# Optimization experiments

Hardware: AMD Instinct MI355X
Metric: run time of the kernel (lower is better)

Reference implementation:

```python
import jax, jax.numpy as jnp
import numpy as np

CONF_THRESH = 0.01
TOP_K = 200        # per-class NMS candidate cap
NMS_THRESH = 0.45
KEEP_TOP_K = 200   # global per-image cap; also output K
TEMPERATURE = 1.0
V0, V1 = 0.1, 0.2  # variances


def _nms_keep(bxs, scs):
    """Greedy NMS over candidates sorted descending by score.
    bxs: [M,4] (x1,y1,x2,y2), scs: [M] (invalid slots have score -1).
    Returns keep mask [M] (bool). Matches torch nm_suppression: a box j is
    suppressed by kept box i iff NOT (IoU(i,j) <= thresh) (NaN IoU suppresses)."""
    x1, y1, x2, y2 = bxs[:, 0], bxs[:, 1], bxs[:, 2], bxs[:, 3]
    area = (x2 - x1) * (y2 - y1)
    xx1 = jnp.maximum(x1[:, None], x1[None, :])
    yy1 = jnp.maximum(y1[:, None], y1[None, :])
    xx2 = jnp.minimum(x2[:, None], x2[None, :])
    yy2 = jnp.minimum(y2[:, None], y2[None, :])
    inter = jnp.clip(xx2 - xx1, 0.0) * jnp.clip(yy2 - yy1, 0.0)
    union = area[None, :] - inter + area[:, None]  # row i: area[i] + area[j] - inter
    iou = inter / union  # [M,M]
    M = scs.shape[0]
    valid = scs > CONF_THRESH

    def step(active, i):
        k_i = active[i]                                  # kept iff still active (sorted desc)
        sup = k_i & jnp.logical_not(iou[i] <= NMS_THRESH)
        return active & jnp.logical_not(sup), k_i

    _, keep = jax.lax.scan(step, valid, jnp.arange(M))
    return keep


def _forward(loc_data, conf_data, dbox_list):
    B, N, C = conf_data.shape
    M, K = TOP_K, KEEP_TOP_K
    # --- box decode (SSD) ---
    db = dbox_list[None]                                   # [1,N,4]
    cxcy = db[..., :2] + loc_data[..., :2] * V0 * db[..., 2:]
    wh = db[..., 2:] * jnp.exp(loc_data[..., 2:] * V1)
    mins = cxcy - wh * 0.5
    boxes = jnp.clip(jnp.concatenate([mins, mins + wh], -1), 0.0, 1.0)  # [B,N,4]
    # --- class scores ---
    probs = jax.nn.softmax(conf_data / TEMPERATURE, axis=-1)
    sc = jnp.swapaxes(probs[..., 1:], 1, 2)                # [B,C-1,N] (skip background)
    masked = jnp.where(sc > CONF_THRESH, sc, -1.0)
    top_sc, top_idx = jax.lax.top_k(masked, M)             # [B,C-1,M] desc
    cand = jnp.take_along_axis(boxes[:, None], top_idx[..., None], axis=2)  # [B,C-1,M,4]
    # --- per-class greedy NMS ---
    keep = jax.vmap(jax.vmap(_nms_keep))(cand, top_sc)     # [B,C-1,M]
    kept_sc = jnp.where(keep, top_sc, 0.0)
    # --- global keep_top_k across classes (torch topk over concatenated dets) ---
    flat = kept_sc.reshape(B, -1)
    order = jnp.argsort(-flat, axis=1)
    rank = jnp.argsort(order, axis=1)                      # inverse permutation = desc rank
    keep_g = (flat > 0.0) & (rank < K)
    fin_sc = jnp.where(keep_g, flat, 0.0).reshape(B, C - 1, M)
    fin_bx = jnp.where(keep_g.reshape(B, C - 1, M)[..., None], cand, 0.0)
    # --- per-class compaction (stable desc sort keeps NMS order among survivors) ---
    ord2 = jnp.argsort(-fin_sc, axis=2)
    sc_out = jnp.take_along_axis(fin_sc, ord2, axis=2)[..., :K]
    bx_out = jnp.take_along_axis(fin_bx, ord2[..., None], axis=2)[..., :K, :]
    body = jnp.concatenate([sc_out[..., None], bx_out], axis=-1)  # [B,C-1,K,5]
    bg = jnp.zeros((B, 1, K, 5), body.dtype)               # class 0 (background) row stays 0
    return jnp.concatenate([bg, body], axis=1)             # [B,C,K,5]


def setup_inputs() -> dict:
    key = jax.random.key(0)
    k1, k2, k3 = jax.random.split(key, 3)
    B, N, C = 8, 32768, 81
    loc_data = jax.random.normal(k1, (B, N, 4), jnp.float32)
    conf_data = jax.random.normal(k2, (B, N, C), jnp.float32)
    dbox_list = jax.random.uniform(k3, (N, 4), jnp.float32, 0.05, 0.95)  # cx,cy,w,h priors
    return {"loc_data": loc_data, "conf_data": conf_data, "dbox_list": dbox_list}


def reference(loc_data, conf_data, dbox_list):
    return _forward(loc_data, conf_data, dbox_list)
```

## Files before the change

kernel.cpp:

```cpp
#include <hip/hip_runtime.h>
#include <stdint.h>

#define CONF_T 0.01f
#define NMS_T  0.45f
#define M_TOP  200
#define TK_BS  512
#define TCAP   2048

typedef float float4u __attribute__((ext_vector_type(4), aligned(4)));

__device__ __forceinline__ uint32_t fkey(float f) {
    uint32_t u = __float_as_uint(f);
    return (u & 0x80000000u) ? ~u : (u | 0x80000000u);
}
__device__ __forceinline__ float fkey_inv(uint32_t k) {
    uint32_t u = (k & 0x80000000u) ? (k & 0x7FFFFFFFu) : ~k;
    return __uint_as_float(u);
}

__device__ __forceinline__ void suffix_select(
        uint32_t* hist, uint32_t* wsum, int nb, uint32_t pref, int shift,
        uint32_t wantv, uint32_t* s_prefix, uint32_t* s_want) {
    int tid = threadIdx.x;
    int lane = tid & 63, w = tid >> 6;
    int bpt = nb >> 8;
    int base = tid * bpt;
    uint32_t loc = 0, sfx = 0;
    if (tid < 256) {
        for (int j = 0; j < bpt; j++) loc += hist[base + j];
        sfx = loc;
        #pragma unroll
        for (int d = 1; d < 64; d <<= 1) {
            uint32_t y = __shfl_down(sfx, d);
            if (lane + d < 64) sfx += y;
        }
        if (lane == 0) wsum[w] = sfx;
    }
    __syncthreads();
    if (tid < 256) {
        uint32_t later = 0;
        for (int j = w + 1; j < 4; j++) later += wsum[j];
        uint32_t run = (sfx - loc) + later;
        for (int j = bpt - 1; j >= 0; j--) {
            uint32_t h = hist[base + j];
            uint32_t s2 = run + h;
            if (run < wantv && s2 >= wantv) {
                *s_prefix = pref | ((uint32_t)(base + j) << shift);
                *s_want   = wantv - run;
            }
            run = s2;
        }
    }
    __syncthreads();
}

__device__ __forceinline__ void suffix_select2(
        uint32_t* hist, uint32_t* wsum, int nb, uint32_t want_a, uint32_t want_b,
        uint32_t* s_bin_a, uint32_t* s_bin_b) {
    int tid = threadIdx.x;
    int lane = tid & 63, w = tid >> 6;
    int bpt = nb >> 8;
    int base = tid * bpt;
    uint32_t loc = 0, sfx = 0;
    if (tid < 256) {
        for (int j = 0; j < bpt; j++) loc += hist[base + j];
        sfx = loc;
        #pragma unroll
        for (int d = 1; d < 64; d <<= 1) {
            uint32_t y = __shfl_down(sfx, d);
            if (lane + d < 64) sfx += y;
        }
        if (lane == 0) wsum[w] = sfx;
    }
    __syncthreads();
    if (tid < 256) {
        uint32_t later = 0;
        for (int j = w + 1; j < 4; j++) later += wsum[j];
        uint32_t run = (sfx - loc) + later;
        for (int j = bpt - 1; j >= 0; j--) {
            uint32_t h = hist[base + j];
            uint32_t s2 = run + h;
            if (run < want_a && s2 >= want_a) *s_bin_a = (uint32_t)(base + j);
            if (run < want_b && s2 >= want_b) *s_bin_b = (uint32_t)(base + j);
            run = s2;
        }
    }
    __syncthreads();
}

__device__ __forceinline__ float4 decode_box(float4 l, float4 d) {
    float cx = d.x + (l.x * 0.1f) * d.z;
    float cy = d.y + (l.y * 0.1f) * d.w;
    float w  = d.z * expf(l.z * 0.2f);
    float h  = d.w * expf(l.w * 0.2f);
    float x1 = cx - w * 0.5f, y1 = cy - h * 0.5f;
    float x2 = x1 + w, y2 = y1 + h;
    float4 o;
    o.x = fminf(fmaxf(x1, 0.f), 1.f);
    o.y = fminf(fmaxf(y1, 0.f), 1.f);
    o.z = fminf(fmaxf(x2, 0.f), 1.f);
    o.w = fminf(fmaxf(y2, 0.f), 1.f);
    return o;
}

__global__ __launch_bounds__(256, 4) void softmax_kernel(
        const float* __restrict__ conf, float* __restrict__ sc,
        int* __restrict__ pcnt, int B, int N, int C) {
    int r = blockIdx.x * blockDim.x + threadIdx.x;
    if (r < B) pcnt[r] = 0;
    if (r >= B * N) return;
    const float* p = conf + (size_t)r * 81;
    float v[81];
    #pragma unroll
    for (int i = 0; i < 20; i++) {
        float4u f = *(const float4u*)(p + 4 * i);
        v[4 * i] = f.x; v[4 * i + 1] = f.y; v[4 * i + 2] = f.z; v[4 * i + 3] = f.w;
    }
    v[80] = p[80];
    float m = v[0];
    #pragma unroll
    for (int c = 1; c < 81; c++) m = fmaxf(m, v[c]);
    float s = 0.f;
    #pragma unroll
    for (int c = 0; c < 81; c++) { float e = expf(v[c] - m); v[c] = e; s += e; }
    int b = r / N, n = r % N;
    float* obase = sc + ((size_t)b * (C - 1)) * N + n;
    #pragma unroll
    for (int c = 1; c < 81; c++) obase[(size_t)(c - 1) * N] = v[c] / s;
}

__global__ __launch_bounds__(TK_BS) void topk_kernel(
        const float* __restrict__ sc, const float* __restrict__ loc,
        const float* __restrict__ dbox,
        float* __restrict__ cand,
        float* __restrict__ cmpval, int* __restrict__ cmpidx,
        int* __restrict__ pcnt,
        int B, int N, int Cm1, int M) {
    const uint32_t KEYN1 = 0x407FFFFFu;
    const uint32_t BIN_N1 = KEYN1 >> 21;
    __shared__ __align__(16) uint32_t hist[2048];
    __shared__ __align__(16) uint32_t tk[TCAP];
    __shared__ int      tix[TCAP];
    __shared__ uint32_t wsum[4];
    __shared__ uint32_t s_prefix, s_want, s_bin_a, s_bin_b;
    __shared__ uint32_t ngt, ntie, tcnt;
    __shared__ float    e_val[256];
    __shared__ int      e_idx[256];
    __shared__ int      tiebuf[256];
    __shared__ float    s_sc[M_TOP];
    __shared__ __align__(16) float4 s_bb[M_TOP];
    __shared__ float    s_ar[M_TOP];

    int row = blockIdx.x;
    int b = row / Cm1, c = row % Cm1;
    int tid = threadIdx.x;
    const float* v = sc + (size_t)row * N;
    const float4* v4 = (const float4*)v;
    int n4 = N >> 2;

    bool sampled = (N >= 2048) && ((N & 3) == 0);
    float loF = 0.f, hiF = 0.f;
    if (sampled) {
        int stride = N >> 2;
        float smp[4];
        #pragma unroll
        for (int s = 0; s < 4; s++) smp[s] = v[s * stride + tid];
        for (int i = tid; i < 2048; i += TK_BS) hist[i] = 0;
        __syncthreads();
        #pragma unroll
        for (int s = 0; s < 4; s++) {
            float f = smp[s];
            atomicAdd(&hist[fkey(f > CONF_T ? f : -1.0f) >> 21], 1u);
        }
        __syncthreads();
        suffix_select2(hist, wsum, 2048, 3u, 25u, &s_bin_a, &s_bin_b);
        uint32_t h = s_bin_a, l = s_bin_b;
        uint32_t hi_key = ((h + 1) << 21) - 1u;
        uint32_t lo_key = (l << 21) - 1u;
        hiF = fkey_inv(hi_key);
        loF = fmaxf(fkey_inv(lo_key), CONF_T);
        sampled = (l > BIN_N1);
    }

    if (tid < 256) { e_val[tid] = -1.0f; e_idx[tid] = tid; }
    if (tid == 0) { ngt = 0; ntie = 0; tcnt = 0; }
    __syncthreads();

    bool ok = false;
    uint32_t G = 0, T = 0;
    if (sampled) {
        for (int i0 = tid; i0 < n4; i0 += 8 * TK_BS) {
            float4 f[8];
            #pragma unroll
            for (int u = 0; u < 8; u++) {
                int i = i0 + u * TK_BS;
                if (i < n4) f[u] = v4[i];
            }
            #pragma unroll
            for (int u = 0; u < 8; u++) {
                int i = i0 + u * TK_BS;
                if (i < n4) {
                    float e[4] = { f[u].x, f[u].y, f[u].z, f[u].w };
                    #pragma unroll
                    for (int j = 0; j < 4; j++) {
                        float fv = e[j];
                        if (fv > loF) {
                            int idx = 4 * i + j;
                            if (fv > hiF) {
                                uint32_t p = atomicAdd(&ngt, 1u);
                                if (p < 256) { e_val[p] = fv; e_idx[p] = idx; }
                            } else {
                                uint32_t p = atomicAdd(&tcnt, 1u);
                                if (p < TCAP) { tk[p] = fkey(fv); tix[p] = idx; }
                            }
                        }
                    }
                }
            }
        }
        for (int i = (n4 << 2) + tid; i < N; i += TK_BS) {
            float fv = v[i];
            if (fv > loF) {
                if (fv > hiF) {
                    uint32_t p = atomicAdd(&ngt, 1u);
                    if (p < 256) { e_val[p] = fv; e_idx[p] = i; }
                } else {
                    uint32_t p = atomicAdd(&tcnt, 1u);
                    if (p < TCAP) { tk[p] = fkey(fv); tix[p] = i; }
                }
            }
        }
        __syncthreads();
        G = ngt; T = tcnt;
        ok = (G <= (uint32_t)M_TOP) && (T <= (uint32_t)TCAP) &&
             (G + T >= (uint32_t)M_TOP);
    }

    uint32_t kth = KEYN1, rfin = 0;
    if (ok) {
        uint32_t want_t = (uint32_t)M_TOP - G;
        if (want_t > 0) {
            for (int i = tid; i < 2048; i += TK_BS) hist[i] = 0;
            __syncthreads();
            for (int i = tid; i < (int)T; i += TK_BS) atomicAdd(&hist[tk[i] >> 21], 1u);
            __syncthreads();
            suffix_select(hist, wsum, 2048, 0u, 21, want_t, &s_prefix, &s_want);
            uint32_t pre0 = s_prefix, w0 = s_want;
            uint32_t bb0 = pre0 >> 21;
            for (int i = tid; i < 2048; i += TK_BS) hist[i] = 0;
            __syncthreads();
            for (int i = tid; i < (int)T; i += TK_BS)
                if ((tk[i] >> 21) == bb0) atomicAdd(&hist[(tk[i] >> 10) & 2047u], 1u);
            __syncthreads();
            suffix_select(hist, wsum, 2048, pre0, 10, w0, &s_prefix, &s_want);
            uint32_t pre1 = s_prefix, w1 = s_want;
            for (int i = tid; i < 1024; i += TK_BS) hist[i] = 0;
            __syncthreads();
            for (int i = tid; i < (int)T; i += TK_BS)
                if ((tk[i] >> 10) == (pre1 >> 10)) atomicAdd(&hist[tk[i] & 1023u], 1u);
            __syncthreads();
            suffix_select(hist, wsum, 1024, pre1, 0, w1, &s_prefix, &s_want);
            kth = s_prefix; rfin = s_want;
            for (int i = tid; i < (int)T; i += TK_BS) {
                uint32_t k = tk[i];
                if (k > kth) {
                    uint32_t p = atomicAdd(&ngt, 1u);
                    if (p < 256) { e_val[p] = fkey_inv(k); e_idx[p] = tix[i]; }
                } else if (k == kth) {
                    uint32_t p = atomicAdd(&ntie, 1u);
                    if (p < 256) tiebuf[p] = tix[i];
                }
            }
            __syncthreads();
        }
    } else {
        if (tid < 256) { e_val[tid] = -1.0f; e_idx[tid] = tid; }
        if (tid == 0) { ngt = 0; ntie = 0; tcnt = 0; }
        for (int i = tid; i < 2048; i += TK_BS) hist[i] = 0;
        __syncthreads();
        for (int i = tid; i < n4; i += TK_BS) {
            float4 f = v4[i];
            atomicAdd(&hist[fkey(f.x > CONF_T ? f.x : -1.0f) >> 21], 1u);
            atomicAdd(&hist[fkey(f.y > CONF_T ? f.y : -1.0f) >> 21], 1u);
            atomicAdd(&hist[fkey(f.z > CONF_T ? f.z : -1.0f) >> 21], 1u);
            atomicAdd(&hist[fkey(f.w > CONF_T ? f.w : -1.0f) >> 21], 1u);
        }
        for (int i = (n4 << 2) + tid; i < N; i += TK_BS)
            atomicAdd(&hist[fkey(v[i] > CONF_T ? v[i] : -1.0f) >> 21], 1u);
        __syncthreads();
        suffix_select(hist, wsum, 2048, 0u, 21, M_TOP, &s_prefix, &s_want);
        uint32_t b0 = s_prefix >> 21;
        uint32_t want1 = s_want;
        bool collect_ties = (b0 != BIN_N1);
        for (int i = tid; i < N; i += TK_BS) {
            float f = v[i];
            float mv = f > CONF_T ? f : -1.0f;
            uint32_t k = fkey(mv);
            uint32_t bin = k >> 21;
            if (bin > b0) {
                uint32_t p = atomicAdd(&ngt, 1u);
                if (p < 256) { e_val[p] = mv; e_idx[p] = i; }
            } else if (bin == b0 && collect_ties) {
                uint32_t p = atomicAdd(&tcnt, 1u);
                if (p < TCAP) { tk[p] = k; tix[p] = i; }
            }
        }
        __syncthreads();
        if (collect_ties && tcnt <= TCAP) {
            int Tl = (int)tcnt;
            for (int i = tid; i < 2048; i += TK_BS) hist[i] = 0;
            __syncthreads();
            for (int i = tid; i < Tl; i += TK_BS) atomicAdd(&hist[(tk[i] >> 10) & 2047u], 1u);
            __syncthreads();
            suffix_select(hist, wsum, 2048, b0 << 21, 10, want1, &s_prefix, &s_want);
            uint32_t pre2 = s_prefix; uint32_t want2 = s_want;
            uint32_t b1 = (pre2 >> 10) & 2047u;
            for (int i = tid; i < 1024; i += TK_BS) hist[i] = 0;
            __syncthreads();
            for (int i = tid; i < Tl; i += TK_BS)
                if (((tk[i] >> 10) & 2047u) == b1) atomicAdd(&hist[tk[i] & 1023u], 1u);
            __syncthreads();
            suffix_select(hist, wsum, 1024, pre2, 0, want2, &s_prefix, &s_want);
            kth = s_prefix; rfin = s_want;
            for (int i = tid; i < Tl; i += TK_BS) {
                uint32_t k = tk[i];
                if (k > kth) {
                    uint32_t p = atomicAdd(&ngt, 1u);
                    if (p < 256) { e_val[p] = fkey_inv(k); e_idx[p] = tix[i]; }
                } else if (k == kth) {
                    uint32_t p = atomicAdd(&ntie, 1u);
                    if (p < 256) tiebuf[p] = tix[i];
                }
            }
            __syncthreads();
        } else if (collect_ties) {
            const int shifts[2] = {10, 0};
            const int nbins_[2] = {2048, 1024};
            if (tid == 0) { s_prefix = b0 << 21; s_want = want1; }
            __syncthreads();
            for (int lev = 0; lev < 2; lev++) {
                int shift = shifts[lev];
                int nb = nbins_[lev];
                uint32_t bmask = (uint32_t)nb - 1u;
                uint32_t pref = s_prefix, wantv = s_want;
                uint32_t pmask = 0xFFFFFFFFu << (shift + ((nb == 2048) ? 11 : 10));
                for (int i = tid; i < nb; i += TK_BS) hist[i] = 0;
                __syncthreads();
                for (int i = tid; i < N; i += TK_BS) {
                    float f = v[i];
                    uint32_t k = fkey(f > CONF_T ? f : -1.0f);
                    if ((k & pmask) == (pref & pmask)) atomicAdd(&hist[(k >> shift) & bmask], 1u);
                }
                __syncthreads();
                suffix_select(hist, wsum, nb, pref, shift, wantv, &s_prefix, &s_want);
            }
            kth = s_prefix; rfin = s_want;
            for (int i = tid; i < N; i += TK_BS) {
                float f = v[i];
                float mv = f > CONF_T ? f : -1.0f;
                uint32_t k = fkey(mv);
                if ((k >> 21) == b0) {
                    if (k > kth) {
                        uint32_t p = atomicAdd(&ngt, 1u);
                        if (p < 256) { e_val[p] = mv; e_idx[p] = i; }
                    } else if (k == kth) {
                        uint32_t p = atomicAdd(&ntie, 1u);
                        if (p < 256) tiebuf[p] = i;
                    }
                }
            }
            __syncthreads();
        }
    }

    uint32_t gcount = min(ngt, (uint32_t)M_TOP);
    uint32_t nt = min(ntie, 256u);
    if (tid < (int)nt) {
        int mine = tiebuf[tid];
        uint32_t rk = 0;
        for (uint32_t j = 0; j < nt; j++) if (tiebuf[j] < mine) rk++;
        if (rk < rfin) {
            uint32_t slot = gcount + rk;
            if (slot < M_TOP) { e_val[slot] = fkey_inv(kth); e_idx[slot] = mine; }
        }
    }
    __syncthreads();
    uint64_t* e_pack = (uint64_t*)tk;
    if (tid < 256)
        e_pack[tid] = ((uint64_t)fkey(e_val[tid]) << 32) | (uint32_t)~(uint32_t)e_idx[tid];
    __syncthreads();
    if (tid < M_TOP) {
        uint64_t mine = e_pack[tid];
        uint32_t rk = 0;
        for (int j = 0; j < M_TOP; j++) rk += (e_pack[j] > mine) ? 1u : 0u;
        float mv = e_val[tid]; int mi = e_idx[tid];
        float4 l = ((const float4*)loc)[(size_t)b * N + mi];
        float4 d = ((const float4*)dbox)[mi];
        float4 bx = decode_box(l, d);
        ((float4*)cand)[(size_t)row * M_TOP + rk] = bx;
        s_sc[rk] = mv;
        s_bb[rk] = bx;
        s_ar[rk] = (bx.z - bx.x) * (bx.w - bx.y);
    }
    __syncthreads();

    uint64_t* sup = (uint64_t*)hist;
    for (int task = tid; task < M_TOP * 4; task += TK_BS) {
        int i = task >> 2, w = task & 3;
        float4 bi = s_bb[i];
        float ai = s_ar[i];
        int jb = w << 6;
        int jn = M_TOP - jb; if (jn > 64) jn = 64;
        uint64_t m = 0;
        for (int j = 0; j < jn; j++) {
            float4 bj = s_bb[jb + j];
            float xx1 = fmaxf(bi.x, bj.x);
            float yy1 = fmaxf(bi.y, bj.y);
            float xx2 = fminf(bi.z, bj.z);
            float yy2 = fminf(bi.w, bj.w);
            float inter = fmaxf(xx2 - xx1, 0.f) * fmaxf(yy2 - yy1, 0.f);
            float uni = (s_ar[jb + j] - inter) + ai;
            float iou = inter / uni;
            if (!(iou <= NMS_T)) m |= (1ull << j);
        }
        sup[(i << 2) + w] = m;
    }
    __syncthreads();

    if (tid < 64) {
        int lane = tid;
        uint64_t act[4], keep[4];
        #pragma unroll
        for (int s = 0; s < 4; s++) {
            int j = (s << 6) + lane;
            float sv = (j < M_TOP) ? s_sc[j] : -1.0f;
            act[s] = __ballot(sv > CONF_T);
            keep[s] = 0;
        }
        #pragma unroll
        for (int s = 0; s < 4; s++) {
            int lim = M_TOP - (s << 6); if (lim > 64) lim = 64;
            for (int bi2 = 0; bi2 < lim; bi2++) {
                if ((act[s] >> bi2) & 1ull) {
                    keep[s] |= (1ull << bi2);
                    int i4 = ((s << 6) + bi2) << 2;
                    act[0] &= ~sup[i4 + 0];
                    act[1] &= ~sup[i4 + 1];
                    act[2] &= ~sup[i4 + 2];
                    act[3] &= ~sup[i4 + 3];
                }
            }
        }
        int total = 0;
        #pragma unroll
        for (int s = 0; s < 4; s++) total += (int)__popcll(keep[s]);
        int base = 0;
        if (lane == 0 && total > 0) base = atomicAdd(&pcnt[b], total);
        base = __shfl(base, 0);
        unsigned long long lower = (lane == 0) ? 0ull : (~0ull >> (64 - lane));
        int off = base;
        #pragma unroll
        for (int s = 0; s < 4; s++) {
            if ((keep[s] >> lane) & 1ull) {
                int pos = off + (int)__popcll(keep[s] & lower);
                cmpval[(size_t)b * M + pos] = s_sc[(s << 6) + lane];
                cmpidx[(size_t)b * M + pos] = c * M_TOP + (s << 6) + lane;
            }
            off += (int)__popcll(keep[s]);
        }
    }
}

#define GT_BS 1024
__global__ __launch_bounds__(GT_BS) void gtop_kernel(
        const float* __restrict__ cmpval, const int* __restrict__ cmpidx,
        const int* __restrict__ pcnt, float* __restrict__ gl_val,
        int* __restrict__ gl_idx, int* __restrict__ gl_cnt, int M) {
    int b = blockIdx.x;
    int tid = threadIdx.x;
    int P = pcnt[b];
    const float* cv = cmpval + (size_t)b * M;
    const int*   ci = cmpidx + (size_t)b * M;
    if (P <= M_TOP) {
        for (int i = tid; i < P; i += GT_BS) {
            gl_val[b * M_TOP + i] = cv[i];
            gl_idx[b * M_TOP + i] = ci[i];
        }
        if (tid == 0) gl_cnt[b] = P;
        return;
    }
    __shared__ uint32_t hist[256];
    __shared__ uint32_t s_prefix, s_want;
    __shared__ int tiebuf[256];
    __shared__ uint32_t ntie, wcnt;
    __shared__ int cutoff;
    if (tid == 0) { s_prefix = 0; s_want = M_TOP; }
    for (int pass = 0; pass < 4; pass++) {
        if (tid < 256) hist[tid] = 0;
        __syncthreads();
        uint32_t prefix = s_prefix;
        int shift = 24 - 8 * pass;
        for (int i = tid; i < P; i += GT_BS) {
            uint32_t k = fkey(cv[i]);
            bool ok = (pass == 0) || ((k >> (shift + 8)) == (prefix >> (shift + 8)));
            if (ok) atomicAdd(&hist[(k >> shift) & 255u], 1u);
        }
        __syncthreads();
        if (tid == 0) {
            uint32_t want = s_want, cum = 0; int bin = 0;
            for (int bb = 255; bb >= 0; bb--) {
                if (cum + hist[bb] >= want) { bin = bb; break; }
                cum += hist[bb];
            }
            s_want = want - cum;
            s_prefix = prefix | ((uint32_t)bin << shift);
        }
        __syncthreads();
    }
    uint32_t kth = s_prefix, rfin = s_want;
    if (tid == 0) { ntie = 0; cutoff = -1; wcnt = 0; }
    __syncthreads();
    for (int i = tid; i < P; i += GT_BS) {
        if (fkey(cv[i]) == kth) { uint32_t p = atomicAdd(&ntie, 1u); if (p < 256) tiebuf[p] = ci[i]; }
    }
    __syncthreads();
    uint32_t nt = min(ntie, 256u);
    if (tid < (int)nt) {
        int mine = tiebuf[tid];
        uint32_t rk = 0;
        for (uint32_t j = 0; j < nt; j++) if (tiebuf[j] < mine) rk++;
        if (rk == rfin - 1) cutoff = mine;
    }
    __syncthreads();
    int cut = cutoff;
    for (int i = tid; i < P; i += GT_BS) {
        uint32_t k = fkey(cv[i]);
        if (k > kth || (k == kth && ci[i] <= cut)) {
            uint32_t p = atomicAdd(&wcnt, 1u);
            gl_val[b * M_TOP + p] = cv[i];
            gl_idx[b * M_TOP + p] = ci[i];
        }
    }
    if (tid == 0) gl_cnt[b] = M_TOP;
}

__global__ __launch_bounds__(256) void out_kernel(
        const float* __restrict__ gl_val, const int* __restrict__ gl_idx,
        const int* __restrict__ gl_cnt, const float* __restrict__ cand,
        float* __restrict__ out, int C, int Cm1) {
    int row = blockIdx.x;
    int b = row / C, cc = row % C;
    int tid = threadIdx.x;
    size_t oslab = (size_t)row * M_TOP * 5;
    if (cc == 0) {
        float4 z; z.x = 0.f; z.y = 0.f; z.z = 0.f; z.w = 0.f;
        float4* o4 = (float4*)(out + oslab);
        for (int i = tid; i < M_TOP * 5 / 4; i += 256) o4[i] = z;
        return;
    }
    int c = cc - 1;
    __shared__ float lv[M_TOP];
    __shared__ int   lm[M_TOP];
    __shared__ uint32_t nloc;
    if (tid == 0) nloc = 0;
    __syncthreads();
    int cnt = gl_cnt[b];
    for (int i = tid; i < cnt; i += 256) {
        int idx = gl_idx[b * M_TOP + i];
        if (idx / M_TOP == c) {
            uint32_t p = atomicAdd(&nloc, 1u);
            lv[p] = gl_val[b * M_TOP + i];
            lm[p] = idx % M_TOP;
        }
    }
    __syncthreads();
    int nc = (int)nloc;
    if (tid < M_TOP) {
        if (tid < nc) {
            float v = lv[tid]; int m = lm[tid];
            int rk = 0;
            for (int j = 0; j < nc; j++)
                if (lv[j] > v || (lv[j] == v && lm[j] < m)) rk++;
            float4 bb = ((const float4*)cand)[((size_t)(b * Cm1 + c)) * M_TOP + m];
            size_t o = oslab + (size_t)rk * 5;
            out[o] = v; out[o + 1] = bb.x; out[o + 2] = bb.y;
            out[o + 3] = bb.z; out[o + 4] = bb.w;
        } else {
            size_t o = oslab + (size_t)tid * 5;
            out[o] = 0.f; out[o + 1] = 0.f; out[o + 2] = 0.f;
            out[o + 3] = 0.f; out[o + 4] = 0.f;
        }
    }
}

extern "C" void kernel_launch(void* const* d_in, const int* in_sizes, int n_in,
                              void* d_out, int out_size, void* d_ws, size_t ws_size,
                              hipStream_t stream) {
    const float* loc  = (const float*)d_in[0];
    const float* conf = (const float*)d_in[1];
    const float* dbox = (const float*)d_in[2];
    int N   = in_sizes[2] / 4;
    int B   = in_sizes[0] / (4 * N);
    int C   = in_sizes[1] / (B * N);
    int Cm1 = C - 1;
    int M   = Cm1 * M_TOP;

    char* ws = (char*)d_ws;
    size_t off = 0;
    auto alloc = [&](size_t bytes) -> char* {
        char* p = ws + off;
        off = (off + bytes + 255) & ~(size_t)255;
        return p;
    };
    float* sc     = (float*)alloc((size_t)B * Cm1 * N * sizeof(float));
    float* cand   = (float*)alloc((size_t)B * M * 4 * sizeof(float));
    int*   pcnt   = (int*)alloc((size_t)B * sizeof(int));
    float* cmpval = (float*)alloc((size_t)B * M * sizeof(float));
    int*   cmpidx = (int*)alloc((size_t)B * M * sizeof(int));
    float* gl_val = (float*)alloc((size_t)B * M_TOP * sizeof(float));
    int*   gl_idx = (int*)alloc((size_t)B * M_TOP * sizeof(int));
    int*   gl_cnt = (int*)alloc((size_t)B * sizeof(int));

    int bn = B * N;
    softmax_kernel<<<(bn + 255) / 256, 256, 0, stream>>>(conf, sc, pcnt, B, N, C);
    topk_kernel<<<B * Cm1, TK_BS, 0, stream>>>(sc, loc, dbox, cand, cmpval, cmpidx, pcnt,
                                               B, N, Cm1, M);
    gtop_kernel<<<B, GT_BS, 0, stream>>>(cmpval, cmpidx, pcnt, gl_val, gl_idx, gl_cnt, M);
    out_kernel<<<B * C, 256, 0, stream>>>(gl_val, gl_idx, gl_cnt, cand, (float*)d_out, C, Cm1);
}
```

Before: 268.5 us.

## Split top-k selection and NMS into separate kernels with transposed suppression masks

The fused top-k+NMS kernel becomes two kernels: a selection kernel that writes sorted top-200 scores and indices to global memory, and a 256-thread NMS kernel that decodes boxes and runs greedy suppression. The suppression matrix is now built transposed, so each lane holds its own column bits, and the serial greedy loop uses a wave ballot over per-lane alive flags instead of shared-memory mask reads. The selection scan's load unroll also goes from 8 to 16 float4s per thread. This frees the selection kernel from NMS shared memory and registers, which may raise occupancy, at the cost of an extra launch and a global round trip for candidates.

```diff
diff --git a/kernel.cpp b/kernel.cpp
--- a/kernel.cpp
+++ b/kernel.cpp
@@ -5,6 +5,7 @@
 #define NMS_T  0.45f
 #define M_TOP  200
 #define TK_BS  512
+#define NMS_BS 256
 #define TCAP   2048
 
 typedef float float4u __attribute__((ext_vector_type(4), aligned(4)));
@@ -129,13 +130,10 @@
     for (int c = 1; c < 81; c++) obase[(size_t)(c - 1) * N] = v[c] / s;
 }
 
-__global__ __launch_bounds__(TK_BS) void topk_kernel(
-        const float* __restrict__ sc, const float* __restrict__ loc,
-        const float* __restrict__ dbox,
-        float* __restrict__ cand,
-        float* __restrict__ cmpval, int* __restrict__ cmpidx,
-        int* __restrict__ pcnt,
-        int B, int N, int Cm1, int M) {
+__global__ __launch_bounds__(TK_BS) void sel_kernel(
+        const float* __restrict__ sc,
+        float* __restrict__ tval, int* __restrict__ tidx,
+        int B, int N, int Cm1) {
     const uint32_t KEYN1 = 0x407FFFFFu;
     const uint32_t BIN_N1 = KEYN1 >> 21;
     __shared__ __align__(16) uint32_t hist[2048];
@@ -147,12 +145,8 @@
     __shared__ float    e_val[256];
     __shared__ int      e_idx[256];
     __shared__ int      tiebuf[256];
-    __shared__ float    s_sc[M_TOP];
-    __shared__ __align__(16) float4 s_bb[M_TOP];
-    __shared__ float    s_ar[M_TOP];
 
     int row = blockIdx.x;
-    int b = row / Cm1, c = row % Cm1;
     int tid = threadIdx.x;
     const float* v = sc + (size_t)row * N;
     const float4* v4 = (const float4*)v;
@@ -189,15 +183,15 @@
     bool ok = false;
     uint32_t G = 0, T = 0;
     if (sampled) {
-        for (int i0 = tid; i0 < n4; i0 += 8 * TK_BS) {
-            float4 f[8];
+        for (int i0 = tid; i0 < n4; i0 += 16 * TK_BS) {
+            float4 f[16];
             #pragma unroll
-            for (int u = 0; u < 8; u++) {
+            for (int u = 0; u < 16; u++) {
                 int i = i0 + u * TK_BS;
                 if (i < n4) f[u] = v4[i];
             }
             #pragma unroll
-            for (int u = 0; u < 8; u++) {
+            for (int u = 0; u < 16; u++) {
                 int i = i0 + u * TK_BS;
                 if (i < n4) {
                     float e[4] = { f[u].x, f[u].y, f[u].z, f[u].w };
@@ -393,67 +387,100 @@
         uint64_t mine = e_pack[tid];
         uint32_t rk = 0;
         for (int j = 0; j < M_TOP; j++) rk += (e_pack[j] > mine) ? 1u : 0u;
-        float mv = e_val[tid]; int mi = e_idx[tid];
+        tval[(size_t)row * M_TOP + rk] = e_val[tid];
+        tidx[(size_t)row * M_TOP + rk] = e_idx[tid];
+    }
+}
+
+__global__ __launch_bounds__(NMS_BS) void nms_kernel(
+        const float* __restrict__ tval, const int* __restrict__ tidx,
+        const float* __restrict__ loc, const float* __restrict__ dbox,
+        float* __restrict__ cand,
+        float* __restrict__ cmpval, int* __restrict__ cmpidx,
+        int* __restrict__ pcnt,
+        int B, int N, int Cm1, int M) {
+    __shared__ __align__(16) float4 s_bb[M_TOP];
+    __shared__ float    s_ar[M_TOP];
+    __shared__ float    s_sc[M_TOP];
+    __shared__ __align__(16) uint64_t supT[M_TOP * 4];
+
+    int row = blockIdx.x;
+    int b = row / Cm1, c = row % Cm1;
+    int tid = threadIdx.x;
+
+    if (tid < M_TOP) {
+        float mv = tval[(size_t)row * M_TOP + tid];
+        int   mi = tidx[(size_t)row * M_TOP + tid];
         float4 l = ((const float4*)loc)[(size_t)b * N + mi];
         float4 d = ((const float4*)dbox)[mi];
         float4 bx = decode_box(l, d);
-        ((float4*)cand)[(size_t)row * M_TOP + rk] = bx;
-        s_sc[rk] = mv;
-        s_bb[rk] = bx;
-        s_ar[rk] = (bx.z - bx.x) * (bx.w - bx.y);
-    }
-    __syncthreads();
-
-    uint64_t* sup = (uint64_t*)hist;
-    for (int task = tid; task < M_TOP * 4; task += TK_BS) {
-        int i = task >> 2, w = task & 3;
-        float4 bi = s_bb[i];
-        float ai = s_ar[i];
-        int jb = w << 6;
-        int jn = M_TOP - jb; if (jn > 64) jn = 64;
+        ((float4*)cand)[(size_t)row * M_TOP + tid] = bx;
+        s_sc[tid] = mv;
+        s_bb[tid] = bx;
+        s_ar[tid] = (bx.z - bx.x) * (bx.w - bx.y);
+    }
+    __syncthreads();
+
+    for (int t = tid; t < M_TOP * 4; t += NMS_BS) {
+        int iw = t / M_TOP;
+        int j  = t - iw * M_TOP;
+        float4 bj = s_bb[j];
+        float arJ = s_ar[j];
+        int i0 = iw << 6;
+        int iN = M_TOP - i0; if (iN > 64) iN = 64; if (iN < 0) iN = 0;
         uint64_t m = 0;
-        for (int j = 0; j < jn; j++) {
-            float4 bj = s_bb[jb + j];
+        for (int k = 0; k < iN; k++) {
+            float4 bi = s_bb[i0 + k];
             float xx1 = fmaxf(bi.x, bj.x);
             float yy1 = fmaxf(bi.y, bj.y);
             float xx2 = fminf(bi.z, bj.z);
             float yy2 = fminf(bi.w, bj.w);
             float inter = fmaxf(xx2 - xx1, 0.f) * fmaxf(yy2 - yy1, 0.f);
-            float uni = (s_ar[jb + j] - inter) + ai;
+            float uni = (arJ - inter) + s_ar[i0 + k];
             float iou = inter / uni;
-            if (!(iou <= NMS_T)) m |= (1ull << j);
-        }
-        sup[(i << 2) + w] = m;
+            if (!(iou <= NMS_T)) m |= (1ull << k);
+        }
+        supT[(j << 2) + iw] = m;
     }
     __syncthreads();
 
     if (tid < 64) {
         int lane = tid;
-        uint64_t act[4], keep[4];
+        uint64_t st0[4], st1[4], st2[4], st3[4];
+        bool alive[4]; int keepb[4];
         #pragma unroll
         for (int s = 0; s < 4; s++) {
             int j = (s << 6) + lane;
-            float sv = (j < M_TOP) ? s_sc[j] : -1.0f;
-            act[s] = __ballot(sv > CONF_T);
-            keep[s] = 0;
-        }
-        #pragma unroll
-        for (int s = 0; s < 4; s++) {
-            int lim = M_TOP - (s << 6); if (lim > 64) lim = 64;
-            for (int bi2 = 0; bi2 < lim; bi2++) {
-                if ((act[s] >> bi2) & 1ull) {
-                    keep[s] |= (1ull << bi2);
-                    int i4 = ((s << 6) + bi2) << 2;
-                    act[0] &= ~sup[i4 + 0];
-                    act[1] &= ~sup[i4 + 1];
-                    act[2] &= ~sup[i4 + 2];
-                    act[3] &= ~sup[i4 + 3];
+            bool inb = (j < M_TOP);
+            uint64_t w0 = inb ? supT[(j << 2) + 0] : 0ull;
+            uint64_t w1 = inb ? supT[(j << 2) + 1] : 0ull;
+            uint64_t w2 = inb ? supT[(j << 2) + 2] : 0ull;
+            uint64_t w3 = inb ? supT[(j << 2) + 3] : 0ull;
+            if (s == 0) { st0[0]=w0; st0[1]=w1; st0[2]=w2; st0[3]=w3; }
+            if (s == 1) { st1[0]=w0; st1[1]=w1; st1[2]=w2; st1[3]=w3; }
+            if (s == 2) { st2[0]=w0; st2[1]=w1; st2[2]=w2; st2[3]=w3; }
+            if (s == 3) { st3[0]=w0; st3[1]=w1; st3[2]=w2; st3[3]=w3; }
+            alive[s] = inb ? (s_sc[j] > CONF_T) : false;
+            keepb[s] = 0;
+        }
+        #pragma unroll
+        for (int iw = 0; iw < 4; iw++) {
+            int lim = M_TOP - (iw << 6); if (lim > 64) lim = 64; if (lim < 0) lim = 0;
+            for (int b2 = 0; b2 < lim; b2++) {
+                uint64_t mask = __ballot(alive[iw]);
+                if ((mask >> b2) & 1ull) {
+                    if (lane == b2) keepb[iw] = 1;
+                    alive[0] = alive[0] && !((st0[iw] >> b2) & 1ull);
+                    alive[1] = alive[1] && !((st1[iw] >> b2) & 1ull);
+                    alive[2] = alive[2] && !((st2[iw] >> b2) & 1ull);
+                    alive[3] = alive[3] && !((st3[iw] >> b2) & 1ull);
                 }
             }
         }
+        unsigned long long ball[4];
         int total = 0;
         #pragma unroll
-        for (int s = 0; s < 4; s++) total += (int)__popcll(keep[s]);
+        for (int s = 0; s < 4; s++) { ball[s] = __ballot(keepb[s] != 0); total += (int)__popcll(ball[s]); }
         int base = 0;
         if (lane == 0 && total > 0) base = atomicAdd(&pcnt[b], total);
         base = __shfl(base, 0);
@@ -461,12 +488,12 @@
         int off = base;
         #pragma unroll
         for (int s = 0; s < 4; s++) {
-            if ((keep[s] >> lane) & 1ull) {
-                int pos = off + (int)__popcll(keep[s] & lower);
+            if (keepb[s]) {
+                int pos = off + (int)__popcll(ball[s] & lower);
                 cmpval[(size_t)b * M + pos] = s_sc[(s << 6) + lane];
                 cmpidx[(size_t)b * M + pos] = c * M_TOP + (s << 6) + lane;
             }
-            off += (int)__popcll(keep[s]);
+            off += (int)__popcll(ball[s]);
         }
     }
 }
@@ -620,11 +647,14 @@
     float* gl_val = (float*)alloc((size_t)B * M_TOP * sizeof(float));
     int*   gl_idx = (int*)alloc((size_t)B * M_TOP * sizeof(int));
     int*   gl_cnt = (int*)alloc((size_t)B * sizeof(int));
+    float* tval   = (float*)alloc((size_t)B * Cm1 * M_TOP * sizeof(float));
+    int*   tidx   = (int*)alloc((size_t)B * Cm1 * M_TOP * sizeof(int));
 
     int bn = B * N;
     softmax_kernel<<<(bn + 255) / 256, 256, 0, stream>>>(conf, sc, pcnt, B, N, C);
-    topk_kernel<<<B * Cm1, TK_BS, 0, stream>>>(sc, loc, dbox, cand, cmpval, cmpidx, pcnt,
-                                               B, N, Cm1, M);
+    sel_kernel<<<B * Cm1, TK_BS, 0, stream>>>(sc, tval, tidx, B, N, Cm1);
+    nms_kernel<<<B * Cm1, NMS_BS, 0, stream>>>(tval, tidx, loc, dbox, cand,
+                                               cmpval, cmpidx, pcnt, B, N, Cm1, M);
     gtop_kernel<<<B, GT_BS, 0, stream>>>(cmpval, cmpidx, pcnt, gl_val, gl_idx, gl_cnt, M);
     out_kernel<<<B * C, 256, 0, stream>>>(gl_val, gl_idx, gl_cnt, cand, (float*)d_out, C, Cm1);
 }
```

Measured after the change: 278.7 us. 3.8% more time.
